# Performance work log

Hardware: AMD Instinct MI355X
Metric: run time of the kernel (lower is better)

Reference implementation:

```python
import jax, jax.numpy as jnp
import numpy as np
from math import sqrt

I = 1024  # input_size
H = 1024  # hidden_size
B = 4096  # batch


def setup_inputs() -> dict:
    key = jax.random.key(0)
    ks = jax.random.split(key, 12)
    a = 1.0 / sqrt(H)
    u = lambda k, shape: jax.random.uniform(k, shape, jnp.float32, -a, a)
    return {
        "x": jax.random.normal(ks[0], (B, I), jnp.float32),
        "hx": jax.random.normal(ks[1], (B, H), jnp.float32),
        "cx": jax.random.normal(ks[2], (B, H), jnp.float32),
        "weight_ih": u(ks[3], (4 * H, I)),
        "weight_hh": u(ks[4], (4 * H, H)),
        "bias_ih": u(ks[5], (4 * H,)),
        "bias_hh": u(ks[6], (4 * H,)),
        "W_peephole_i": u(ks[7], (H, H)),
        "W_peephole_f": u(ks[8], (H, H)),
        "W_peephole_o": u(ks[9], (H, H)),
    }


def reference(x, hx, cx, weight_ih, weight_hh, bias_ih, bias_hh,
              W_peephole_i, W_peephole_f, W_peephole_o):
    # gates: [B, 4H]
    gates = x @ weight_ih.T + bias_ih + hx @ weight_hh.T + bias_hh
    ingate, forgetgate, cellgate, outgate = jnp.split(gates, 4, axis=1)
    # F.linear(cx, W * eye) == cx * diag(W)  (diagonal peephole)
    ingate = jax.nn.sigmoid(ingate + cx * jnp.diagonal(W_peephole_i))
    forgetgate = jax.nn.sigmoid(forgetgate + cx * jnp.diagonal(W_peephole_f))
    cellgate = jnp.tanh(cellgate)
    cy = forgetgate * cx + ingate * cellgate
    # NOTE: original code reuses W_peephole_f for the output gate (faithful to source)
    outgate = jax.nn.sigmoid(outgate + cy * jnp.diagonal(W_peephole_f))
    hy = outgate * jnp.tanh(cy)
    return (hy, cy)
```

## Files before the change

### kernel.cpp

```cpp
#include <hip/hip_runtime.h>
#include <cstdint>


namespace {

constexpr int H   = 1024;
constexpr int K2  = 2048;
constexpr int BSZ = 4096;
constexpr size_t OUT_CY = (size_t)BSZ * H;

typedef __attribute__((ext_vector_type(8))) short bf16x8;
typedef __attribute__((ext_vector_type(4))) float f32x4;
typedef __attribute__((ext_vector_type(8))) unsigned short u16x8;

__device__ __forceinline__ unsigned short f2bf(float f) {
  union { float f; uint32_t u; } v; v.f = f;
  uint32_t u = v.u;
  u += 0x7FFFu + ((u >> 16) & 1u);
  return (unsigned short)(u >> 16);
}

__device__ __forceinline__ float sigm(float x) {
  return 1.0f / (1.0f + __expf(-x));
}
__device__ __forceinline__ float tanh_fast(float x) {
  return 1.0f - 2.0f / (1.0f + __expf(2.0f * x));
}

__device__ __forceinline__ void gload_lds16(const void* g, void* l) {
  __builtin_amdgcn_global_load_lds(
      (const __attribute__((address_space(1))) void*)g,
      (__attribute__((address_space(3))) void*)l, 16, 0, 0);
}

__device__ __forceinline__ bf16x8 dsr_b128(unsigned addr) {
  bf16x8 r;
  asm volatile("ds_read_b128 %0, %1" : "=v"(r) : "v"(addr));
  return r;
}

}

__global__ __launch_bounds__(256) void cast_kernel(
    const float* __restrict__ x, const float* __restrict__ hx,
    const float* __restrict__ wih, const float* __restrict__ whh,
    unsigned short* __restrict__ A, unsigned short* __restrict__ W) {
  int b = blockIdx.x;
  bool isW = b >= 4096;
  int t = (isW ? b - 4096 : b) * 256 + threadIdx.x;
  int idx = t * 8;
  int n = idx >> 11;
  int k = idx & 2047;
  const float* s0 = isW ? wih : x;
  const float* s1 = isW ? whh : hx;
  const float* src = (k < H) ? (s0 + (size_t)n * H + k)
                             : (s1 + (size_t)n * H + (k - H));
  float4 v0 = *(const float4*)src;
  float4 v1 = *(const float4*)(src + 4);
  u16x8 o;
  o[0] = f2bf(v0.x); o[1] = f2bf(v0.y); o[2] = f2bf(v0.z); o[3] = f2bf(v0.w);
  o[4] = f2bf(v1.x); o[5] = f2bf(v1.y); o[6] = f2bf(v1.z); o[7] = f2bf(v1.w);
  if (isW) {
    int g = n >> 10, hh = n & 1023;
    int np = ((hh >> 4) << 6) + (g << 4) + (hh & 15);
    *(u16x8*)(W + (size_t)np * K2 + k) = o;
  } else {
    *(u16x8*)(A + (size_t)idx) = o;
  }
}

__global__ __launch_bounds__(512, 2) void lstm_fused_gemm(
    const unsigned short* __restrict__ A,
    const unsigned short* __restrict__ W,
    const float* __restrict__ cx,
    const float* __restrict__ bias_ih, const float* __restrict__ bias_hh,
    const float* __restrict__ Wpi, const float* __restrict__ Wpf,
    float* __restrict__ out) {
  __shared__ __align__(16) unsigned short lds[2 * 32768];

  const int tid  = threadIdx.x;
  const int lane = tid & 63;
  const int wave = tid >> 6;
  const int wm   = wave >> 2;
  const int wn   = wave & 3;

  const int b   = blockIdx.y * 16 + blockIdx.x;
  const int xcd = b & 7, idx = b >> 3;
  const int bx  = (xcd & 3) * 4 + (idx & 3);
  const int by  = (xcd >> 2) * 8 + (idx >> 2);
  const int m0 = bx * 256;
  const int w0 = by * 256;

  const int srow   = tid >> 3;
  const int schunk = ((tid & 7) ^ (srow & 7)) << 3;

  const int col  = lane & 15;
  const int quad = lane >> 4;

  const unsigned short* Asrc = A + (size_t)(m0 + srow) * K2 + schunk;
  const unsigned short* Wsrc = W + (size_t)(w0 + srow) * K2 + schunk;
  const int ldsdst = wave * 512;

  f32x4 acc[8][4];
#pragma unroll
  for (int i = 0; i < 8; ++i)
#pragma unroll
    for (int j = 0; j < 4; ++j)
      acc[i][j] = (f32x4){0.f, 0.f, 0.f, 0.f};

  auto stA = [&](int kt, int buf, int p) {
    gload_lds16(Asrc + (size_t)p * 64 * K2 + kt * 64,
                &lds[buf * 32768 + p * 4096 + ldsdst]);
  };
  auto stB = [&](int kt, int buf, int p) {
    gload_lds16(Wsrc + (size_t)p * 64 * K2 + kt * 64,
                &lds[buf * 32768 + 16384 + p * 4096 + ldsdst]);
  };

#pragma unroll
  for (int p = 0; p < 4; ++p) stA(0, 0, p);
#pragma unroll
  for (int p = 0; p < 4; ++p) stB(0, 0, p);
#pragma unroll
  for (int p = 0; p < 4; ++p) stA(1, 1, p);
#pragma unroll
  for (int p = 0; p < 4; ++p) stB(1, 1, p);
  asm volatile("s_waitcnt vmcnt(8)" ::: "memory");
  __builtin_amdgcn_sched_barrier(0);
  __builtin_amdgcn_s_barrier();

  const unsigned lds0 = (unsigned)(size_t)(__attribute__((address_space(3))) char*)lds;
  const unsigned abase = lds0 + (unsigned)((wm * 128 + col) * 128);
  const unsigned bbase = lds0 + 32768u + (unsigned)((wn * 64 + col) * 128);
  const unsigned kch0 = ((quad ^ (col & 7)) << 4);
  const unsigned kch1 = (((4 + quad) ^ (col & 7)) << 4);

#pragma unroll 2
  for (int kt = 0; kt < 32; ++kt) {
    const int buf = kt & 1;
    const unsigned boffs = (unsigned)(buf * 65536);
    const bool pf = (kt + 2 < 32);
    bf16x8 bfr[4][2];
#pragma unroll
    for (int q = 0; q < 4; ++q) {
      bf16x8 afr[2][2];
      if (q == 0) {
#pragma unroll
        for (int j = 0; j < 4; ++j) {
          bfr[j][0] = dsr_b128(bbase + boffs + j * 2048 + kch0);
          bfr[j][1] = dsr_b128(bbase + boffs + j * 2048 + kch1);
        }
      }
#pragma unroll
      for (int i2 = 0; i2 < 2; ++i2) {
        afr[i2][0] = dsr_b128(abase + boffs + (2 * q + i2) * 2048 + kch0);
        afr[i2][1] = dsr_b128(abase + boffs + (2 * q + i2) * 2048 + kch1);
      }
      if (q == 1 && pf) { stB(kt + 2, buf, 0); stB(kt + 2, buf, 1); }
      if (q == 2 && pf) { stB(kt + 2, buf, 2); stB(kt + 2, buf, 3); }
      if (q == 3 && pf) { stA(kt + 2, buf, 0); stA(kt + 2, buf, 2); }
      __builtin_amdgcn_s_barrier();
      asm volatile("s_waitcnt lgkmcnt(0)" ::: "memory");
      __builtin_amdgcn_sched_barrier(0);
      __builtin_amdgcn_s_setprio(1);
#pragma unroll
      for (int i2 = 0; i2 < 2; ++i2)
#pragma unroll
        for (int j = 0; j < 4; ++j)
          acc[2 * q + i2][j] = __builtin_amdgcn_mfma_f32_16x16x32_bf16(
              afr[i2][0], bfr[j][0], acc[2 * q + i2][j], 0, 0, 0);
#pragma unroll
      for (int i2 = 0; i2 < 2; ++i2)
#pragma unroll
        for (int j = 0; j < 4; ++j)
          acc[2 * q + i2][j] = __builtin_amdgcn_mfma_f32_16x16x32_bf16(
              afr[i2][1], bfr[j][1], acc[2 * q + i2][j], 0, 0, 0);
      __builtin_amdgcn_s_setprio(0);
      __builtin_amdgcn_s_barrier();
    }
    if (pf) {
      stA(kt + 2, buf, 1); stA(kt + 2, buf, 3);
      asm volatile("s_waitcnt vmcnt(8)" ::: "memory");
    } else {
      asm volatile("s_waitcnt vmcnt(0)" ::: "memory");
    }
    __builtin_amdgcn_sched_barrier(0);
    __builtin_amdgcn_s_barrier();
  }

  const int h = by * 64 + wn * 16 + col;
  const float bi  = bias_ih[h]         + bias_hh[h];
  const float bf_ = bias_ih[H + h]     + bias_hh[H + h];
  const float bc  = bias_ih[2 * H + h] + bias_hh[2 * H + h];
  const float bo  = bias_ih[3 * H + h] + bias_hh[3 * H + h];
  const float di = Wpi[(size_t)h * (H + 1)];
  const float df = Wpf[(size_t)h * (H + 1)];
  const int mbase = m0 + wm * 128 + quad * 4;
#pragma unroll
  for (int i = 0; i < 8; ++i) {
#pragma unroll
    for (int r = 0; r < 4; ++r) {
      const int m = mbase + i * 16 + r;
      const float c  = cx[(size_t)m * H + h];
      const float ip = acc[i][0][r] + bi;
      const float fp = acc[i][1][r] + bf_;
      const float cp = acc[i][2][r] + bc;
      const float op = acc[i][3][r] + bo;
      const float ig = sigm(ip + c * di);
      const float fg = sigm(fp + c * df);
      const float cg = tanh_fast(cp);
      const float cy = fg * c + ig * cg;
      const float og = sigm(op + cy * df);
      const float hy = og * tanh_fast(cy);
      out[(size_t)m * H + h] = hy;
      out[OUT_CY + (size_t)m * H + h] = cy;
    }
  }
}

extern "C" void kernel_launch(void* const* d_in, const int* in_sizes, int n_in,
                              void* d_out, int out_size, void* d_ws, size_t ws_size,
                              hipStream_t stream) {
  const float* x   = (const float*)d_in[0];
  const float* hx  = (const float*)d_in[1];
  const float* cx  = (const float*)d_in[2];
  const float* wih = (const float*)d_in[3];
  const float* whh = (const float*)d_in[4];
  const float* bih = (const float*)d_in[5];
  const float* bhh = (const float*)d_in[6];
  const float* wpi = (const float*)d_in[7];
  const float* wpf = (const float*)d_in[8];
  float* out = (float*)d_out;

  unsigned short* Abf = (unsigned short*)d_ws;
  unsigned short* Wbf = Abf + (size_t)BSZ * K2;

  cast_kernel<<<8192, 256, 0, stream>>>(x, hx, wih, whh, Abf, Wbf);

  dim3 grid(BSZ / 256, (4 * H) / 256);
  lstm_fused_gemm<<<grid, 512, 0, stream>>>(Abf, Wbf, cx, bih, bhh, wpi, wpf, out);
}
```

Baseline: 203.1 us.

## Software-pipeline LDS fragment reads with double-buffered B registers and fewer barriers

```diff
diff --git a/kernel.cpp b/kernel.cpp
--- a/kernel.cpp
+++ b/kernel.cpp
@@ -69,6 +69,28 @@
   }
 }
 
+#define RD_A(AF, Q, BO)                                          \
+  AF[0][0] = dsr_b128(abase + (BO) + (2 * (Q) + 0) * 2048 + kch0); \
+  AF[0][1] = dsr_b128(abase + (BO) + (2 * (Q) + 0) * 2048 + kch1); \
+  AF[1][0] = dsr_b128(abase + (BO) + (2 * (Q) + 1) * 2048 + kch0); \
+  AF[1][1] = dsr_b128(abase + (BO) + (2 * (Q) + 1) * 2048 + kch1);
+
+#define MFMA_PH(Q, AF, BC)                                                   \
+  __builtin_amdgcn_s_setprio(1);                                             \
+  _Pragma("unroll") for (int i2 = 0; i2 < 2; ++i2)                           \
+      _Pragma("unroll") for (int j = 0; j < 4; ++j)                          \
+          acc[2 * (Q) + i2][j] = __builtin_amdgcn_mfma_f32_16x16x32_bf16(    \
+              AF[i2][0], BC[j][0], acc[2 * (Q) + i2][j], 0, 0, 0);           \
+  _Pragma("unroll") for (int i2 = 0; i2 < 2; ++i2)                           \
+      _Pragma("unroll") for (int j = 0; j < 4; ++j)                          \
+          acc[2 * (Q) + i2][j] = __builtin_amdgcn_mfma_f32_16x16x32_bf16(    \
+              AF[i2][1], BC[j][1], acc[2 * (Q) + i2][j], 0, 0, 0);           \
+  __builtin_amdgcn_s_setprio(0);
+
+#define LGKM(N)                                          \
+  asm volatile("s_waitcnt lgkmcnt(" #N ")" ::: "memory"); \
+  __builtin_amdgcn_sched_barrier(0);
+
 __global__ __launch_bounds__(512, 2) void lstm_fused_gemm(
     const unsigned short* __restrict__ A,
     const unsigned short* __restrict__ W,
@@ -85,9 +107,9 @@
   const int wn   = wave & 3;
 
   const int b   = blockIdx.y * 16 + blockIdx.x;
-  const int xcd = b & 7, idx = b >> 3;
-  const int bx  = (xcd & 3) * 4 + (idx & 3);
-  const int by  = (xcd >> 2) * 8 + (idx >> 2);
+  const int xcd = b & 7, bidx = b >> 3;
+  const int bx  = (xcd & 3) * 4 + (bidx & 3);
+  const int by  = (xcd >> 2) * 8 + (bidx >> 2);
   const int m0 = bx * 256;
   const int w0 = by * 256;
 
@@ -117,82 +139,80 @@
                 &lds[buf * 32768 + 16384 + p * 4096 + ldsdst]);
   };
 
-#pragma unroll
-  for (int p = 0; p < 4; ++p) stA(0, 0, p);
-#pragma unroll
-  for (int p = 0; p < 4; ++p) stB(0, 0, p);
-#pragma unroll
-  for (int p = 0; p < 4; ++p) stA(1, 1, p);
-#pragma unroll
-  for (int p = 0; p < 4; ++p) stB(1, 1, p);
-  asm volatile("s_waitcnt vmcnt(8)" ::: "memory");
-  __builtin_amdgcn_sched_barrier(0);
-  __builtin_amdgcn_s_barrier();
-
   const unsigned lds0 = (unsigned)(size_t)(__attribute__((address_space(3))) char*)lds;
   const unsigned abase = lds0 + (unsigned)((wm * 128 + col) * 128);
   const unsigned bbase = lds0 + 32768u + (unsigned)((wn * 64 + col) * 128);
   const unsigned kch0 = ((quad ^ (col & 7)) << 4);
   const unsigned kch1 = (((4 + quad) ^ (col & 7)) << 4);
 
-#pragma unroll 2
-  for (int kt = 0; kt < 32; ++kt) {
+#pragma unroll
+  for (int p = 0; p < 4; ++p) stA(0, 0, p);
+#pragma unroll
+  for (int p = 0; p < 4; ++p) stB(0, 0, p);
+#pragma unroll
+  for (int p = 0; p < 4; ++p) stA(1, 1, p);
+#pragma unroll
+  for (int p = 0; p < 4; ++p) stB(1, 1, p);
+  asm volatile("s_waitcnt vmcnt(8)" ::: "memory");
+  __builtin_amdgcn_sched_barrier(0);
+  __builtin_amdgcn_s_barrier();
+
+  bf16x8 bfrA[4][2], bfrB[4][2];
+#pragma unroll
+  for (int j = 0; j < 4; ++j) {
+    bfrA[j][0] = dsr_b128(bbase + j * 2048 + kch0);
+    bfrA[j][1] = dsr_b128(bbase + j * 2048 + kch1);
+  }
+
+  auto tile = [&](int kt, bf16x8 (&bcur)[4][2], bf16x8 (&bnxt)[4][2]) {
     const int buf = kt & 1;
-    const unsigned boffs = (unsigned)(buf * 65536);
-    const bool pf = (kt + 2 < 32);
-    bf16x8 bfr[4][2];
-#pragma unroll
-    for (int q = 0; q < 4; ++q) {
-      bf16x8 afr[2][2];
-      if (q == 0) {
-#pragma unroll
-        for (int j = 0; j < 4; ++j) {
-          bfr[j][0] = dsr_b128(bbase + boffs + j * 2048 + kch0);
-          bfr[j][1] = dsr_b128(bbase + boffs + j * 2048 + kch1);
-        }
-      }
-#pragma unroll
-      for (int i2 = 0; i2 < 2; ++i2) {
-        afr[i2][0] = dsr_b128(abase + boffs + (2 * q + i2) * 2048 + kch0);
-        afr[i2][1] = dsr_b128(abase + boffs + (2 * q + i2) * 2048 + kch1);
-      }
-      if (q == 1 && pf) { stB(kt + 2, buf, 0); stB(kt + 2, buf, 1); }
-      if (q == 2 && pf) { stB(kt + 2, buf, 2); stB(kt + 2, buf, 3); }
-      if (q == 3 && pf) { stA(kt + 2, buf, 0); stA(kt + 2, buf, 2); }
-      __builtin_amdgcn_s_barrier();
-      asm volatile("s_waitcnt lgkmcnt(0)" ::: "memory");
-      __builtin_amdgcn_sched_barrier(0);
-      __builtin_amdgcn_s_setprio(1);
-#pragma unroll
-      for (int i2 = 0; i2 < 2; ++i2)
-#pragma unroll
-        for (int j = 0; j < 4; ++j)
-          acc[2 * q + i2][j] = __builtin_amdgcn_mfma_f32_16x16x32_bf16(
-              afr[i2][0], bfr[j][0], acc[2 * q + i2][j], 0, 0, 0);
-#pragma unroll
-      for (int i2 = 0; i2 < 2; ++i2)
-#pragma unroll
-        for (int j = 0; j < 4; ++j)
-          acc[2 * q + i2][j] = __builtin_amdgcn_mfma_f32_16x16x32_bf16(
-              afr[i2][1], bfr[j][1], acc[2 * q + i2][j], 0, 0, 0);
-      __builtin_amdgcn_s_setprio(0);
-      __builtin_amdgcn_s_barrier();
-    }
-    if (pf) {
-      stA(kt + 2, buf, 1); stA(kt + 2, buf, 3);
+    const unsigned bo  = (unsigned)(buf * 65536);
+    const unsigned bon = bo ^ 65536u;
+    bf16x8 af0[2][2], af1[2][2];
+    RD_A(af0, 0, bo);
+    RD_A(af1, 1, bo);
+    LGKM(4);
+    MFMA_PH(0, af0, bcur);
+    RD_A(af0, 2, bo);
+    LGKM(4);
+    MFMA_PH(1, af1, bcur);
+    RD_A(af1, 3, bo);
+    LGKM(4);
+    MFMA_PH(2, af0, bcur);
+    LGKM(0);
+    __builtin_amdgcn_s_barrier();
+    if (kt + 2 < 32) {
+      stA(kt + 2, buf, 0); stA(kt + 2, buf, 1);
+      stA(kt + 2, buf, 2); stA(kt + 2, buf, 3);
+      stB(kt + 2, buf, 0); stB(kt + 2, buf, 1);
+      stB(kt + 2, buf, 2); stB(kt + 2, buf, 3);
       asm volatile("s_waitcnt vmcnt(8)" ::: "memory");
     } else {
       asm volatile("s_waitcnt vmcnt(0)" ::: "memory");
     }
     __builtin_amdgcn_sched_barrier(0);
     __builtin_amdgcn_s_barrier();
+    if (kt < 31) {
+#pragma unroll
+      for (int j = 0; j < 4; ++j) {
+        bnxt[j][0] = dsr_b128(bbase + bon + j * 2048 + kch0);
+        bnxt[j][1] = dsr_b128(bbase + bon + j * 2048 + kch1);
+      }
+    }
+    __builtin_amdgcn_sched_barrier(0);
+    MFMA_PH(3, af1, bcur);
+  };
+
+  for (int kt = 0; kt < 32; kt += 2) {
+    tile(kt,     bfrA, bfrB);
+    tile(kt + 1, bfrB, bfrA);
   }
 
   const int h = by * 64 + wn * 16 + col;
   const float bi  = bias_ih[h]         + bias_hh[h];
   const float bf_ = bias_ih[H + h]     + bias_hh[H + h];
   const float bc  = bias_ih[2 * H + h] + bias_hh[2 * H + h];
-  const float bo  = bias_ih[3 * H + h] + bias_hh[3 * H + h];
+  const float bo_ = bias_ih[3 * H + h] + bias_hh[3 * H + h];
   const float di = Wpi[(size_t)h * (H + 1)];
   const float df = Wpf[(size_t)h * (H + 1)];
   const int mbase = m0 + wm * 128 + quad * 4;
@@ -205,7 +225,7 @@
       const float ip = acc[i][0][r] + bi;
       const float fp = acc[i][1][r] + bf_;
       const float cp = acc[i][2][r] + bc;
-      const float op = acc[i][3][r] + bo;
+      const float op = acc[i][3][r] + bo_;
       const float ig = sigm(ip + c * di);
       const float fg = sigm(fp + c * df);
       const float cg = tanh_fast(cp);
```

New measurement: 405.1 us. +99.5%, slower.

## Fuse fp32-to-bf16 cast into GEMM staging via register loads and packed convert

Applied to the files above, without the earlier changes.

```diff
diff --git a/kernel.cpp b/kernel.cpp
--- a/kernel.cpp
+++ b/kernel.cpp
@@ -5,20 +5,11 @@
 namespace {
 
 constexpr int H   = 1024;
-constexpr int K2  = 2048;
 constexpr int BSZ = 4096;
 constexpr size_t OUT_CY = (size_t)BSZ * H;
 
 typedef __attribute__((ext_vector_type(8))) short bf16x8;
 typedef __attribute__((ext_vector_type(4))) float f32x4;
-typedef __attribute__((ext_vector_type(8))) unsigned short u16x8;
-
-__device__ __forceinline__ unsigned short f2bf(float f) {
-  union { float f; uint32_t u; } v; v.f = f;
-  uint32_t u = v.u;
-  u += 0x7FFFu + ((u >> 16) & 1u);
-  return (unsigned short)(u >> 16);
-}
 
 __device__ __forceinline__ float sigm(float x) {
   return 1.0f / (1.0f + __expf(-x));
@@ -27,10 +18,10 @@
   return 1.0f - 2.0f / (1.0f + __expf(2.0f * x));
 }
 
-__device__ __forceinline__ void gload_lds16(const void* g, void* l) {
-  __builtin_amdgcn_global_load_lds(
-      (const __attribute__((address_space(1))) void*)g,
-      (__attribute__((address_space(3))) void*)l, 16, 0, 0);
+__device__ __forceinline__ unsigned cvtpk(float lo, float hi) {
+  unsigned r;
+  asm("v_cvt_pk_bf16_f32 %0, %1, %2" : "=v"(r) : "v"(lo), "v"(hi));
+  return r;
 }
 
 __device__ __forceinline__ bf16x8 dsr_b128(unsigned addr) {
@@ -41,38 +32,28 @@
 
 }
 
-__global__ __launch_bounds__(256) void cast_kernel(
-    const float* __restrict__ x, const float* __restrict__ hx,
-    const float* __restrict__ wih, const float* __restrict__ whh,
-    unsigned short* __restrict__ A, unsigned short* __restrict__ W) {
-  int b = blockIdx.x;
-  bool isW = b >= 4096;
-  int t = (isW ? b - 4096 : b) * 256 + threadIdx.x;
-  int idx = t * 8;
-  int n = idx >> 11;
-  int k = idx & 2047;
-  const float* s0 = isW ? wih : x;
-  const float* s1 = isW ? whh : hx;
-  const float* src = (k < H) ? (s0 + (size_t)n * H + k)
-                             : (s1 + (size_t)n * H + (k - H));
-  float4 v0 = *(const float4*)src;
-  float4 v1 = *(const float4*)(src + 4);
-  u16x8 o;
-  o[0] = f2bf(v0.x); o[1] = f2bf(v0.y); o[2] = f2bf(v0.z); o[3] = f2bf(v0.w);
-  o[4] = f2bf(v1.x); o[5] = f2bf(v1.y); o[6] = f2bf(v1.z); o[7] = f2bf(v1.w);
-  if (isW) {
-    int g = n >> 10, hh = n & 1023;
-    int np = ((hh >> 4) << 6) + (g << 4) + (hh & 15);
-    *(u16x8*)(W + (size_t)np * K2 + k) = o;
-  } else {
-    *(u16x8*)(A + (size_t)idx) = o;
-  }
-}
+#define LGKM0                                           \
+  asm volatile("s_waitcnt lgkmcnt(0)" ::: "memory");    \
+  __builtin_amdgcn_sched_barrier(0);
+
+#define LDU(P, SRC, OFF)                                      \
+  P##a = *(const float4*)((SRC) + (OFF));                     \
+  P##b = *(const float4*)((SRC) + (OFF) + 16);
+
+#define STU(P, DADDR)                                                   \
+  {                                                                     \
+    uint4 o_;                                                           \
+    o_.x = cvtpk(P##a.x, P##a.y); o_.y = cvtpk(P##a.z, P##a.w);         \
+    o_.z = cvtpk(P##b.x, P##b.y); o_.w = cvtpk(P##b.z, P##b.w);         \
+    *(uint4*)((char*)lds + (DADDR)) = o_;                               \
+  }
 
 __global__ __launch_bounds__(512, 2) void lstm_fused_gemm(
-    const unsigned short* __restrict__ A,
-    const unsigned short* __restrict__ W,
+    const float* __restrict__ x,
+    const float* __restrict__ hx,
     const float* __restrict__ cx,
+    const float* __restrict__ wih,
+    const float* __restrict__ whh,
     const float* __restrict__ bias_ih, const float* __restrict__ bias_hh,
     const float* __restrict__ Wpi, const float* __restrict__ Wpf,
     float* __restrict__ out) {
@@ -85,49 +66,33 @@
   const int wn   = wave & 3;
 
   const int b   = blockIdx.y * 16 + blockIdx.x;
-  const int xcd = b & 7, idx = b >> 3;
-  const int bx  = (xcd & 3) * 4 + (idx & 3);
-  const int by  = (xcd >> 2) * 8 + (idx >> 2);
+  const int xcd = b & 7, bidx = b >> 3;
+  const int bx  = (xcd & 3) * 4 + (bidx & 3);
+  const int by  = (xcd >> 2) * 8 + (bidx >> 2);
   const int m0 = bx * 256;
-  const int w0 = by * 256;
-
-  const int srow   = tid >> 3;
-  const int schunk = ((tid & 7) ^ (srow & 7)) << 3;
+
+  const int srow = tid >> 3;
+  const int c8   = tid & 7;
+
+  const int gB = (srow >> 4) & 3;
+  const int hB = by * 64 + (srow & 15);
+  unsigned offA[4], offB[4];
+#pragma unroll
+  for (int p = 0; p < 4; ++p) {
+    offA[p] = (unsigned)((m0 + p * 64 + srow) * 4096 + c8 * 32);
+    offB[p] = (unsigned)(((gB << 10) + hB + p * 16) * 4096 + c8 * 32);
+  }
+  const unsigned wbyte = (unsigned)(srow * 128 + ((c8 ^ (srow & 7)) << 4));
 
   const int col  = lane & 15;
   const int quad = lane >> 4;
 
-  const unsigned short* Asrc = A + (size_t)(m0 + srow) * K2 + schunk;
-  const unsigned short* Wsrc = W + (size_t)(w0 + srow) * K2 + schunk;
-  const int ldsdst = wave * 512;
-
   f32x4 acc[8][4];
 #pragma unroll
   for (int i = 0; i < 8; ++i)
 #pragma unroll
     for (int j = 0; j < 4; ++j)
       acc[i][j] = (f32x4){0.f, 0.f, 0.f, 0.f};
-
-  auto stA = [&](int kt, int buf, int p) {
-    gload_lds16(Asrc + (size_t)p * 64 * K2 + kt * 64,
-                &lds[buf * 32768 + p * 4096 + ldsdst]);
-  };
-  auto stB = [&](int kt, int buf, int p) {
-    gload_lds16(Wsrc + (size_t)p * 64 * K2 + kt * 64,
-                &lds[buf * 32768 + 16384 + p * 4096 + ldsdst]);
-  };
-
-#pragma unroll
-  for (int p = 0; p < 4; ++p) stA(0, 0, p);
-#pragma unroll
-  for (int p = 0; p < 4; ++p) stB(0, 0, p);
-#pragma unroll
-  for (int p = 0; p < 4; ++p) stA(1, 1, p);
-#pragma unroll
-  for (int p = 0; p < 4; ++p) stB(1, 1, p);
-  asm volatile("s_waitcnt vmcnt(8)" ::: "memory");
-  __builtin_amdgcn_sched_barrier(0);
-  __builtin_amdgcn_s_barrier();
 
   const unsigned lds0 = (unsigned)(size_t)(__attribute__((address_space(3))) char*)lds;
   const unsigned abase = lds0 + (unsigned)((wm * 128 + col) * 128);
@@ -135,11 +100,37 @@
   const unsigned kch0 = ((quad ^ (col & 7)) << 4);
   const unsigned kch1 = (((4 + quad) ^ (col & 7)) << 4);
 
+  float4 s0a, s0b, s1a, s1b, s2a, s2b, s3a, s3b;
+
+  {
+    const char* aX = (const char*)x;
+    const char* bX = (const char*)wih;
+#pragma unroll
+    for (int t = 0; t < 2; ++t) {
+      const unsigned bo = (unsigned)(t * 65536);
+      const unsigned ko = (unsigned)(t * 256);
+      LDU(s0, bX, offB[0] + ko); LDU(s1, bX, offB[1] + ko);
+      STU(s0, bo + 32768u + wbyte); STU(s1, bo + 32768u + 8192u + wbyte);
+      LDU(s0, bX, offB[2] + ko); LDU(s1, bX, offB[3] + ko);
+      STU(s0, bo + 32768u + 16384u + wbyte); STU(s1, bo + 32768u + 24576u + wbyte);
+      LDU(s0, aX, offA[0] + ko); LDU(s1, aX, offA[1] + ko);
+      STU(s0, bo + wbyte); STU(s1, bo + 8192u + wbyte);
+      LDU(s0, aX, offA[2] + ko); LDU(s1, aX, offA[3] + ko);
+      STU(s0, bo + 16384u + wbyte); STU(s1, bo + 24576u + wbyte);
+    }
+  }
+  LGKM0;
+  __builtin_amdgcn_s_barrier();
+
 #pragma unroll 2
   for (int kt = 0; kt < 32; ++kt) {
     const int buf = kt & 1;
     const unsigned boffs = (unsigned)(buf * 65536);
     const bool pf = (kt + 2 < 32);
+    const char* aS = (const char*)(kt < 14 ? x : hx);
+    const char* bS = (const char*)(kt < 14 ? wih : whh);
+    const unsigned kOff = (unsigned)((((kt + 2) * 64) & 1023) * 4);
+
     bf16x8 bfr[4][2];
 #pragma unroll
     for (int q = 0; q < 4; ++q) {
@@ -156,12 +147,21 @@
         afr[i2][0] = dsr_b128(abase + boffs + (2 * q + i2) * 2048 + kch0);
         afr[i2][1] = dsr_b128(abase + boffs + (2 * q + i2) * 2048 + kch1);
       }
-      if (q == 1 && pf) { stB(kt + 2, buf, 0); stB(kt + 2, buf, 1); }
-      if (q == 2 && pf) { stB(kt + 2, buf, 2); stB(kt + 2, buf, 3); }
-      if (q == 3 && pf) { stA(kt + 2, buf, 0); stA(kt + 2, buf, 2); }
+      if (q == 0 && pf) { LDU(s0, bS, offB[0] + kOff); LDU(s1, bS, offB[1] + kOff); }
+      if (q == 1 && pf) {
+        LDU(s2, bS, offB[2] + kOff); LDU(s3, bS, offB[3] + kOff);
+        STU(s0, boffs + 32768u + wbyte); STU(s1, boffs + 32768u + 8192u + wbyte);
+      }
+      if (q == 2 && pf) {
+        LDU(s0, aS, offA[0] + kOff); LDU(s1, aS, offA[2] + kOff);
+        STU(s2, boffs + 32768u + 16384u + wbyte); STU(s3, boffs + 32768u + 24576u + wbyte);
+      }
+      if (q == 3 && pf) {
+        LDU(s2, aS, offA[1] + kOff); LDU(s3, aS, offA[3] + kOff);
+        STU(s0, boffs + wbyte); STU(s1, boffs + 16384u + wbyte);
+      }
       __builtin_amdgcn_s_barrier();
-      asm volatile("s_waitcnt lgkmcnt(0)" ::: "memory");
-      __builtin_amdgcn_sched_barrier(0);
+      LGKM0;
       __builtin_amdgcn_s_setprio(1);
 #pragma unroll
       for (int i2 = 0; i2 < 2; ++i2)
@@ -179,10 +179,8 @@
       __builtin_amdgcn_s_barrier();
     }
     if (pf) {
-      stA(kt + 2, buf, 1); stA(kt + 2, buf, 3);
-      asm volatile("s_waitcnt vmcnt(8)" ::: "memory");
-    } else {
-      asm volatile("s_waitcnt vmcnt(0)" ::: "memory");
+      STU(s2, boffs + 8192u + wbyte);
+      STU(s3, boffs + 24576u + wbyte);
     }
     __builtin_amdgcn_sched_barrier(0);
     __builtin_amdgcn_s_barrier();
@@ -192,7 +190,7 @@
   const float bi  = bias_ih[h]         + bias_hh[h];
   const float bf_ = bias_ih[H + h]     + bias_hh[H + h];
   const float bc  = bias_ih[2 * H + h] + bias_hh[2 * H + h];
-  const float bo  = bias_ih[3 * H + h] + bias_hh[3 * H + h];
+  const float bo_ = bias_ih[3 * H + h] + bias_hh[3 * H + h];
   const float di = Wpi[(size_t)h * (H + 1)];
   const float df = Wpf[(size_t)h * (H + 1)];
   const int mbase = m0 + wm * 128 + quad * 4;
@@ -205,7 +203,7 @@
       const float ip = acc[i][0][r] + bi;
       const float fp = acc[i][1][r] + bf_;
       const float cp = acc[i][2][r] + bc;
-      const float op = acc[i][3][r] + bo;
+      const float op = acc[i][3][r] + bo_;
       const float ig = sigm(ip + c * di);
       const float fg = sigm(fp + c * df);
       const float cg = tanh_fast(cp);
@@ -232,11 +230,7 @@
   const float* wpf = (const float*)d_in[8];
   float* out = (float*)d_out;
 
-  unsigned short* Abf = (unsigned short*)d_ws;
-  unsigned short* Wbf = Abf + (size_t)BSZ * K2;
-
-  cast_kernel<<<8192, 256, 0, stream>>>(x, hx, wih, whh, Abf, Wbf);
-
   dim3 grid(BSZ / 256, (4 * H) / 256);
-  lstm_fused_gemm<<<grid, 512, 0, stream>>>(Abf, Wbf, cx, bih, bhh, wpi, wpf, out);
-}
+  lstm_fused_gemm<<<grid, 512, 0, stream>>>(x, hx, cx, wih, whh,
+                                            bih, bhh, wpi, wpf, out);
+}
```

Result: slower. 258.8 us (+27.4%).
